# Optimization experiments

Hardware: AMD Instinct MI355X
Metric: run time of the kernel (lower is better)

The kernel has to match this reference:

```python
import jax, jax.numpy as jnp
import numpy as np

B = 2            # batch size
GRID = 256       # BEV grid H = W
M = 30000        # number of pillars (voxels)
NPTS = 200000    # number of points
IN_C = 16
VOXEL = 0.4      # voxel_size[:2]
PC_MIN = -51.2   # pc_range[:2]
DS = 2           # prod(ds_layer_strides)


def _bn(x, g, b):
    # eval-mode BatchNorm with running_mean=0, running_var=1 (eps absorbed into g)
    return x * g + b


def _conv(x, k, stride):
    # 3x3 conv, padding=1 (spconv SparseConv2d / SubMConv2d with pad k//2), NHWC
    return jax.lax.conv_general_dilated(
        x, k, (stride, stride), ((1, 1), (1, 1)),
        dimension_numbers=('NHWC', 'HWIO', 'NHWC'))


def _active_mask(occ, stride):
    # active output sites of a sparse conv = any active input in the 3x3 receptive field
    pooled = jax.lax.reduce_window(occ, -jnp.inf, jax.lax.max,
                                   (1, 3, 3, 1), (1, stride, stride, 1),
                                   ((0, 0), (1, 1), (1, 1), (0, 0)))
    return (pooled > 0).astype(occ.dtype)


def _forward(features, pfn_w0, pfn_g0, pfn_b0, pfn_w1, pfn_g1, pfn_b1,
             b1_kd, b1_gd, b1_bd, b1_k1, b1_g1, b1_b1, b1_k2, b1_g2, b1_b2,
             b2_kd, b2_gd, b2_bd, b2_k1, b2_g1, b2_b1, b2_k2, b2_g2, b2_b2,
             unq, unq_inv, grid_size):
    # pillar mode: cols 0:2 are xy; convert to (fractional) voxel coordinates
    pos = (features[:, :2] - PC_MIN) / VOXEL  # [N,2] = (px, py)

    # PFN layer 0 (not last): linear(16->16) + BN + ReLU, concat per-pillar max
    h = jax.nn.relu(_bn(features @ pfn_w0, pfn_g0, pfn_b0))            # [N,16]
    hmax = jax.ops.segment_max(h, unq_inv, num_segments=M)             # [M,16]
    h = jnp.concatenate([h, hmax[unq_inv]], axis=1)                    # [N,32]
    # PFN layer 1 (last): linear(32->64) + BN + ReLU
    h = jax.nn.relu(_bn(h @ pfn_w1, pfn_g1, pfn_b1))                   # [N,64]

    # scatter_max pooling points -> pillars
    fv = jax.ops.segment_max(h, unq_inv, num_segments=M)               # [M,64]

    Hn = grid_size
    img = jnp.zeros((B, Hn, Hn, fv.shape[1]), fv.dtype)
    img = img.at[unq[:, 0], unq[:, 1], unq[:, 2]].set(fv)              # dense BEV, NHWC
    occ = jnp.zeros((B, Hn, Hn, 1), fv.dtype)
    occ = occ.at[unq[:, 0], unq[:, 1], unq[:, 2]].set(1.0)

    # block 1: SparseConvBlock(stride=1) + SparseBasicBlock (dense math, masked to active sites)
    occ1 = _active_mask(occ, 1)
    x = jax.nn.relu(_bn(_conv(img, b1_kd, 1), b1_gd, b1_bd)) * occ1
    y = jax.nn.relu(_bn(_conv(x, b1_k1, 1), b1_g1, b1_b1)) * occ1
    y = _bn(_conv(y, b1_k2, 1), b1_g2, b1_b2) * occ1
    x = jax.nn.relu(x + y)

    # block 2: SparseConvBlock(stride=2) + SparseBasicBlock
    occ2 = _active_mask(occ1, 2)
    x = jax.nn.relu(_bn(_conv(x, b2_kd, 2), b2_gd, b2_bd)) * occ2
    y = jax.nn.relu(_bn(_conv(x, b2_k1, 1), b2_g1, b2_b1)) * occ2
    y = _bn(_conv(y, b2_k2, 1), b2_g2, b2_b2) * occ2
    x = jax.nn.relu(x + y)                                             # [B,H/2,W/2,128]

    # bilinear gather at per-point downsampled positions (px -> W axis, py -> H axis)
    bidx = unq[unq_inv, 0]
    px = pos[:, 0] / DS
    py = pos[:, 1] / DS
    Hc, Wc = x.shape[1], x.shape[2]
    x0 = jnp.clip(jnp.floor(px).astype(jnp.int32), 0, Wc - 1)
    x1 = jnp.clip(jnp.floor(px).astype(jnp.int32) + 1, 0, Wc - 1)
    y0 = jnp.clip(jnp.floor(py).astype(jnp.int32), 0, Hc - 1)
    y1 = jnp.clip(jnp.floor(py).astype(jnp.int32) + 1, 0, Hc - 1)
    Ia = x[bidx, y0, x0]
    Ib = x[bidx, y1, x0]
    Ic = x[bidx, y0, x1]
    Id = x[bidx, y1, x1]
    x0f, x1f = x0.astype(px.dtype), x1.astype(px.dtype)
    y0f, y1f = y0.astype(py.dtype), y1.astype(py.dtype)
    wa = ((x1f - px) * (y1f - py))[:, None]
    wb = ((x1f - px) * (py - y0f))[:, None]
    wc = ((px - x0f) * (y1f - py))[:, None]
    wd = ((px - x0f) * (py - y0f))[:, None]
    return Ia * wa + Ib * wb + Ic * wc + Id * wd                       # [N,128]


def setup_inputs() -> dict:
    rng = np.random.default_rng(0)
    d = {}
    d['features'] = jnp.asarray(rng.standard_normal((NPTS, IN_C)).astype(np.float32))
    # unique voxel coords (batch, y, x)
    lin = rng.choice(B * GRID * GRID, size=M, replace=False)
    d['unq'] = jnp.asarray(np.stack([lin // (GRID * GRID), (lin // GRID) % GRID, lin % GRID], 1).astype(np.int32))
    # every pillar gets at least one point
    d['unq_inv'] = jnp.asarray(np.concatenate([np.arange(M), rng.integers(0, M, NPTS - M)]).astype(np.int32))
    d['grid_size'] = GRID

    def w(*s):
        fan = int(np.prod(s[:-1]))
        return jnp.asarray((rng.standard_normal(s) / np.sqrt(fan)).astype(np.float32))

    def g(c):
        return jnp.asarray((0.5 + 0.5 * rng.random(c)).astype(np.float32))

    def bb(c):
        return jnp.asarray((0.1 * rng.standard_normal(c)).astype(np.float32))

    d['pfn_w0'] = w(IN_C, 16); d['pfn_g0'] = g(16); d['pfn_b0'] = bb(16)
    d['pfn_w1'] = w(32, 64);   d['pfn_g1'] = g(64); d['pfn_b1'] = bb(64)
    d['b1_kd'] = w(3, 3, 64, 64);   d['b1_gd'] = g(64);  d['b1_bd'] = bb(64)
    d['b1_k1'] = w(3, 3, 64, 64);   d['b1_g1'] = g(64);  d['b1_b1'] = bb(64)
    d['b1_k2'] = w(3, 3, 64, 64);   d['b1_g2'] = g(64);  d['b1_b2'] = bb(64)
    d['b2_kd'] = w(3, 3, 64, 128);  d['b2_gd'] = g(128); d['b2_bd'] = bb(128)
    d['b2_k1'] = w(3, 3, 128, 128); d['b2_g1'] = g(128); d['b2_b1'] = bb(128)
    d['b2_k2'] = w(3, 3, 128, 128); d['b2_g2'] = g(128); d['b2_b2'] = bb(128)
    return d


def reference(features, unq, unq_inv, grid_size,
              pfn_w0, pfn_g0, pfn_b0, pfn_w1, pfn_g1, pfn_b1,
              b1_kd, b1_gd, b1_bd, b1_k1, b1_g1, b1_b1, b1_k2, b1_g2, b1_b2,
              b2_kd, b2_gd, b2_bd, b2_k1, b2_g1, b2_b1, b2_k2, b2_g2, b2_b2):
    return _forward(features, pfn_w0, pfn_g0, pfn_b0, pfn_w1, pfn_g1, pfn_b1,
                    b1_kd, b1_gd, b1_bd, b1_k1, b1_g1, b1_b1, b1_k2, b1_g2, b1_b2,
                    b2_kd, b2_gd, b2_bd, b2_k1, b2_g1, b2_b1, b2_k2, b2_g2, b2_b2,
                    unq, unq_inv, grid_size)
```

## Files before the change

### kernel.cpp

```cpp
#include <hip/hip_runtime.h>
#include <hip/hip_bf16.h>

#define NPTS    200000
#define MPIL    30000
#define BATCH   2
#define GRID0   256
#define PCMIN   (-51.2f)
#define VOXEL0  (0.4f)
#define NCHUNK  118

#define SLOT_B  ((size_t)16777216)
#define SLOT_F  ((size_t)33554432)

#define W0F 0
#define W1F 256
#define FB1 9216
#define FB2 156672
#define FB3 304128
#define FB4 451584
#define FB5 746496
#define FB6 1336320

#define WS_FLAG 0
#define WS_OCC8 64
#define WS_OCC1 (64 + 131072)
#define WS_OCC2 (64 + 262144)
#define WS_HMAX 393280
#define WS_CNT  2313280
#define WS_OFF  2433280
#define WS_CUR  2553344
#define WS_IDX  2673344
#define WS_LOC  3473344
#define WS_BS   3593344
#define WS_FX   393344

typedef __attribute__((ext_vector_type(8))) short v8s;
typedef __attribute__((ext_vector_type(4))) float f32x4;

static __device__ __forceinline__ float b2f(__hip_bfloat16 v) { return __bfloat162float(v); }
static __device__ __forceinline__ unsigned short f2bbits(float f) {
    __hip_bfloat16 h = __float2bfloat16(f);
    union { __hip_bfloat16 h; unsigned short u; } cv; cv.h = h; return cv.u;
}
static __device__ __forceinline__ float bits2f(unsigned short h) {
    union { unsigned int u; float f; } c; c.u = ((unsigned int)h) << 16; return c.f;
}
static __device__ __forceinline__ float lo2f(unsigned int u) {
    union { unsigned int u; float f; } c; c.u = u << 16; return c.f;
}
static __device__ __forceinline__ float hi2f(unsigned int u) {
    union { unsigned int u; float f; } c; c.u = u & 0xFFFF0000u; return c.f;
}
static __device__ __forceinline__ unsigned int pack2(float a, float b) {
    return (unsigned int)f2bbits(a) | ((unsigned int)f2bbits(b) << 16);
}
static __device__ __forceinline__ void split2(float a, float b, unsigned int& hi, unsigned int& lo) {
    unsigned short ha = f2bbits(a), hb = f2bbits(b);
    hi = (unsigned int)ha | ((unsigned int)hb << 16);
    float ra = a - bits2f(ha);
    float rb = b - bits2f(hb);
    lo = (unsigned int)f2bbits(ra) | ((unsigned int)f2bbits(rb) << 16);
}

static __device__ __forceinline__ float ldf(const void* p, size_t i, int isb) {
    return isb ? b2f(((const __hip_bfloat16*)p)[i]) : ((const float*)p)[i];
}
static __device__ __forceinline__ float4 ld4(const void* p, size_t i, int isb) {
    if (isb) {
        uint2 r = *(const uint2*)((const __hip_bfloat16*)p + i);
        return make_float4(lo2f(r.x), hi2f(r.x), lo2f(r.y), hi2f(r.y));
    }
    return *(const float4*)((const float*)p + i);
}
static __device__ __forceinline__ void st4(void* p, size_t i, int isb, float4 v) {
    if (isb) {
        uint2 pk; pk.x = pack2(v.x, v.y); pk.y = pack2(v.z, v.w);
        *(uint2*)((__hip_bfloat16*)p + i) = pk;
    } else {
        *(float4*)((float*)p + i) = v;
    }
}
static __device__ __forceinline__ void* actptr(void* ob, int slot, int isb) {
    return (char*)ob + (size_t)slot * (isb ? SLOT_B : SLOT_F);
}
static __device__ __forceinline__ float* wpool(void* ob, int isb) {
    return (float*)((char*)ob + 3 * (isb ? SLOT_B : SLOT_F));
}

__global__ void probe_kernel(const unsigned short* __restrict__ g0, int* __restrict__ flag) {
    if (threadIdx.x == 0 && blockIdx.x == 0) {
        int ok = 1;
        for (int i = 0; i < 8; i++) {
            unsigned short u = g0[i];
            if (u < 0x3E00 || u >= 0x4000) ok = 0;
        }
        *flag = ok;
    }
}

__global__ __launch_bounds__(256) void cvt_kernel(const void* __restrict__ src, void* ob,
                                                  int woff, int n, const int* __restrict__ flag) {
    int isb = *flag;
    int i = blockIdx.x * 256 + threadIdx.x;
    if (i < n) wpool(ob, isb)[woff + i] = ldf(src, i, isb);
}

__global__ __launch_bounds__(256) void wfrag_kernel(const void* __restrict__ src, void* ob,
                                                    int fb_bytes, int CIN, int COUT,
                                                    const int* __restrict__ flag)
{
    const int isb = *flag;
    const int cnt = 9 * CIN * COUT;
    int e = blockIdx.x * 256 + threadIdx.x;
    if (e >= cnt) return;
    int i = e & 7;
    int l = (e >> 3) & 63;
    int f = e >> 9;
    int nbn = COUT >> 4, kcn = CIN >> 5;
    int nb = f % nbn;
    int kc = (f / nbn) % kcn;
    int tap = f / (nbn * kcn);
    int ci = kc * 32 + (l >> 4) * 8 + i;
    int co = nb * 16 + (l & 15);
    float wv = ldf(src, (size_t)(tap * CIN + ci) * COUT + co, isb);
    unsigned short h = f2bbits(wv);
    float rem = wv - bits2f(h);
    short* wh = (short*)((char*)ob + 3 * (isb ? SLOT_B : SLOT_F) + fb_bytes);
    wh[e] = (short)h;
    wh[cnt + e] = (short)f2bbits(rem);
}

__global__ __launch_bounds__(256) void hist_kernel(const int* __restrict__ unq_inv,
                                                   int* __restrict__ cnt)
{
    int n = blockIdx.x * 256 + threadIdx.x;
    if (n < NPTS) atomicAdd(&cnt[unq_inv[n]], 1);
}

__global__ __launch_bounds__(256) void scan1_kernel(const int* __restrict__ cnt,
                                                    int* __restrict__ loc,
                                                    int* __restrict__ bs)
{
    __shared__ int s[256];
    const int tid = threadIdx.x;
    const int i = blockIdx.x * 256 + tid;
    int v = (i < MPIL) ? cnt[i] : 0;
    s[tid] = v;
    __syncthreads();
#pragma unroll
    for (int d = 1; d < 256; d <<= 1) {
        int t = (tid >= d) ? s[tid - d] : 0;
        __syncthreads();
        s[tid] += t;
        __syncthreads();
    }
    if (i < MPIL) loc[i] = s[tid] - v;
    if (tid == 255) bs[blockIdx.x] = s[255];
}

__global__ __launch_bounds__(128) void scan2_kernel(int* __restrict__ bs)
{
    __shared__ int s[NCHUNK];
    const int tid = threadIdx.x;
    for (int i = tid; i < NCHUNK; i += 128) s[i] = bs[i];
    __syncthreads();
    if (tid == 0) {
        int acc = 0;
        for (int i = 0; i < NCHUNK; i++) { int t = s[i]; s[i] = acc; acc += t; }
    }
    __syncthreads();
    for (int i = tid; i < NCHUNK; i += 128) bs[i] = s[i];
}

__global__ __launch_bounds__(256) void scan3_kernel(const int* __restrict__ loc,
                                                    const int* __restrict__ bs,
                                                    int* __restrict__ off,
                                                    int* __restrict__ cur)
{
    int i = blockIdx.x * 256 + threadIdx.x;
    if (i < MPIL) {
        int e = loc[i] + bs[blockIdx.x];
        off[i] = e; cur[i] = e;
    }
    if (i == 0) off[MPIL] = NPTS;
}

__global__ __launch_bounds__(256) void fill_kernel(const int* __restrict__ unq_inv,
                                                   int* __restrict__ cur,
                                                   int* __restrict__ idxarr)
{
    int n = blockIdx.x * 256 + threadIdx.x;
    if (n >= NPTS) return;
    int p = unq_inv[n];
    int s = atomicAdd(&cur[p], 1);
    idxarr[s] = n;
}

__global__ __launch_bounds__(256) void pfn0_kernel(
    const void* __restrict__ feat, void* ob, const void* __restrict__ g0,
    const void* __restrict__ b0, const int* __restrict__ flag)
{
    const int isb = *flag;
    int n = blockIdx.x * 256 + threadIdx.x;
    if (n >= NPTS) return;
    const float* w0f = wpool(ob, isb) + W0F;
    void* h0 = actptr(ob, 1, isb);
    float f[16];
#pragma unroll
    for (int i = 0; i < 16; i += 4) {
        float4 v = ld4(feat, (size_t)n * 16 + i, isb);
        f[i] = v.x; f[i + 1] = v.y; f[i + 2] = v.z; f[i + 3] = v.w;
    }
#pragma unroll
    for (int co = 0; co < 16; co += 4) {
        float a0 = 0.f, a1 = 0.f, a2 = 0.f, a3 = 0.f;
#pragma unroll
        for (int ci = 0; ci < 16; ci++) {
            float4 w = *(const float4*)&w0f[ci * 16 + co];
            a0 += f[ci] * w.x; a1 += f[ci] * w.y; a2 += f[ci] * w.z; a3 += f[ci] * w.w;
        }
        float o[4] = { a0, a1, a2, a3 };
#pragma unroll
        for (int k = 0; k < 4; k++) {
            float z = o[k] * ldf(g0, co + k, isb) + ldf(b0, co + k, isb);
            o[k] = fmaxf(z, 0.f);
        }
        st4(h0, (size_t)n * 16 + co, isb, make_float4(o[0], o[1], o[2], o[3]));
    }
}

__global__ __launch_bounds__(256) void hmax_kernel(
    void* ob, const int* __restrict__ off, const int* __restrict__ idxarr,
    float* __restrict__ hmax, const int* __restrict__ flag)
{
    const int isb = *flag;
    int t = blockIdx.x * 256 + threadIdx.x;
    if (t >= MPIL * 16) return;
    int p = t >> 4, ch = t & 15;
    const void* h0 = actptr(ob, 1, isb);
    float m = 0.f;
    int s1 = off[p + 1];
    for (int s = off[p]; s < s1; s++) {
        int n = idxarr[s];
        m = fmaxf(m, ldf(h0, (size_t)n * 16 + ch, isb));
    }
    hmax[t] = m;
}

template<bool BF>
static __device__ __forceinline__ void pfn1p_body(
    void* ob, const float* __restrict__ hmax, const void* __restrict__ g1,
    const void* __restrict__ b1, const int* __restrict__ off,
    const int* __restrict__ idxarr, const int* __restrict__ unq,
    unsigned char* __restrict__ occ)
{
    const int lane = threadIdx.x & 63;
    const int p = (blockIdx.x << 2) + (threadIdx.x >> 6);
    if (p >= MPIL) return;
    const int isb = BF ? 1 : 0;
    const float* w1f = wpool(ob, isb) + W1F;
    const void* h0 = actptr(ob, 1, isb);
    void* img = actptr(ob, 0, isb);

    float wcol[32];
#pragma unroll
    for (int k = 0; k < 32; k++) wcol[k] = w1f[k * 64 + lane];
    float base = 0.f;
#pragma unroll
    for (int k = 0; k < 16; k++) base += hmax[(size_t)p * 16 + k] * wcol[16 + k];
    const float g = ldf(g1, lane, isb);
    const float be = ldf(b1, lane, isb);

    float m = 0.f;
    const int s1 = off[p + 1];
    for (int s = off[p]; s < s1; s++) {
        const int n = idxarr[s];
        float h[16];
        if (BF) {
            const unsigned short* hp = (const unsigned short*)h0 + (size_t)n * 16;
            uint4 a = *(const uint4*)hp;
            uint4 c = *(const uint4*)(hp + 8);
            h[0] = lo2f(a.x); h[1] = hi2f(a.x); h[2] = lo2f(a.y); h[3] = hi2f(a.y);
            h[4] = lo2f(a.z); h[5] = hi2f(a.z); h[6] = lo2f(a.w); h[7] = hi2f(a.w);
            h[8] = lo2f(c.x); h[9] = hi2f(c.x); h[10] = lo2f(c.y); h[11] = hi2f(c.y);
            h[12] = lo2f(c.z); h[13] = hi2f(c.z); h[14] = lo2f(c.w); h[15] = hi2f(c.w);
        } else {
            const float* fp = (const float*)h0 + (size_t)n * 16;
#pragma unroll
            for (int i = 0; i < 16; i += 4) {
                float4 v = *(const float4*)(fp + i);
                h[i] = v.x; h[i + 1] = v.y; h[i + 2] = v.z; h[i + 3] = v.w;
            }
        }
        float z = base;
#pragma unroll
        for (int k = 0; k < 16; k++) z += h[k] * wcol[k];
        z = fmaxf(z * g + be, 0.f);
        m = fmaxf(m, z);
    }

    const int bb = unq[p * 3 + 0], yy = unq[p * 3 + 1], xx = unq[p * 3 + 2];
    const size_t site = ((size_t)bb * GRID0 + yy) * GRID0 + xx;
    if (BF) ((unsigned short*)img)[site * 64 + lane] = f2bbits(m);
    else    ((float*)img)[site * 64 + lane] = m;
    if (lane == 0) occ[site] = 1;
}

__global__ __launch_bounds__(256) void pfn1p_kernel(
    void* ob, const float* __restrict__ hmax, const void* __restrict__ g1,
    const void* __restrict__ b1, const int* __restrict__ off,
    const int* __restrict__ idxarr, const int* __restrict__ unq,
    unsigned char* __restrict__ occ, const int* __restrict__ flag)
{
    if (*flag) pfn1p_body<true>(ob, hmax, g1, b1, off, idxarr, unq, occ);
    else       pfn1p_body<false>(ob, hmax, g1, b1, off, idxarr, unq, occ);
}

__global__ __launch_bounds__(256) void dilate1_kernel(const unsigned char* __restrict__ occ,
                                                      unsigned char* __restrict__ occ1)
{
    int idx = blockIdx.x * 256 + threadIdx.x;
    if (idx >= BATCH * GRID0 * GRID0) return;
    int b = idx / (GRID0 * GRID0);
    int r = idx % (GRID0 * GRID0);
    int y = r / GRID0, x = r % GRID0;
    unsigned char v = 0;
#pragma unroll
    for (int dy = -1; dy <= 1; dy++) {
        int yy = y + dy; if (yy < 0 || yy >= GRID0) continue;
#pragma unroll
        for (int dx = -1; dx <= 1; dx++) {
            int xx = x + dx; if (xx < 0 || xx >= GRID0) continue;
            v |= occ[((size_t)b * GRID0 + yy) * GRID0 + xx];
        }
    }
    occ1[idx] = v ? 1 : 0;
}

__global__ __launch_bounds__(256) void dilate2_kernel(const unsigned char* __restrict__ occ1,
                                                      unsigned char* __restrict__ occ2)
{
    int idx = blockIdx.x * 256 + threadIdx.x;
    if (idx >= BATCH * 128 * 128) return;
    int b = idx / (128 * 128);
    int r = idx % (128 * 128);
    int y = r / 128, x = r % 128;
    unsigned char v = 0;
#pragma unroll
    for (int dy = -1; dy <= 1; dy++) {
        int yy = 2 * y + dy; if (yy < 0 || yy >= GRID0) continue;
#pragma unroll
        for (int dx = -1; dx <= 1; dx++) {
            int xx = 2 * x + dx; if (xx < 0 || xx >= GRID0) continue;
            v |= occ1[((size_t)b * GRID0 + yy) * GRID0 + xx];
        }
    }
    occ2[idx] = v ? 1 : 0;
}

template<int CIN, int COUT, int STRIDE, bool ADD_RES, bool BF, int RT, int WC, int WP, int CSPLIT>
static __device__ __forceinline__ void conv_tile(
    short* s_a, const void* in, void* outp, const void* res, const short* wh,
    const void* gamma, const void* beta, const unsigned char* mask,
    int HIN, int WIN, int HOUT, int WOUT, int b, int oy0, int ox0, int nbB)
{
    constexpr int Y_EXT = (RT - 1) * STRIDE + 3;
    constexpr int X_EXT = 15 * STRIDE + 3;
    constexpr int TSZ = Y_EXT * X_EXT * CIN;
    constexpr int NCH8 = CIN / 8;
    constexpr int RPW = RT / WP;
    constexpr int CG = COUT / 16 / CSPLIT / WC;
    constexpr int KCN = CIN / 32;
    constexpr int KCNT = 9 * KCN;
    constexpr int CP = 3;
    constexpr int NPASS = KCNT / CP;
    constexpr int NOB = COUT / 16;

    const int tid = threadIdx.x;

    __syncthreads();
    for (int i = tid; i < Y_EXT * X_EXT * NCH8; i += 256) {
        int c8 = i % NCH8;
        int r = i / NCH8;
        int xo = r % X_EXT;
        int dy = r / X_EXT;
        int yin = oy0 * STRIDE - 1 + dy;
        int xin = ox0 * STRIDE - 1 + xo;
        bool inb = (yin >= 0 && yin < HIN && xin >= 0 && xin < WIN);
        int si = (dy * X_EXT + xo) * CIN + ((c8 ^ (xo & 7)) << 3);
        size_t gi = (((size_t)b * HIN + yin) * WIN + xin) * (size_t)CIN + c8 * 8;
        if (BF) {
            uint4 v = make_uint4(0u, 0u, 0u, 0u);
            if (inb) v = *(const uint4*)((const unsigned short*)in + gi);
            *(uint4*)&s_a[si] = v;
        } else {
            float4 va = make_float4(0.f, 0.f, 0.f, 0.f);
            float4 vb = make_float4(0.f, 0.f, 0.f, 0.f);
            if (inb) {
                va = *(const float4*)((const float*)in + gi);
                vb = *(const float4*)((const float*)in + gi + 4);
            }
            uint4 hv, lv;
            split2(va.x, va.y, hv.x, lv.x);
            split2(va.z, va.w, hv.y, lv.y);
            split2(vb.x, vb.y, hv.z, lv.z);
            split2(vb.z, vb.w, hv.w, lv.w);
            *(uint4*)&s_a[si] = hv;
            *(uint4*)&s_a[TSZ + si] = lv;
        }
    }
    __syncthreads();

    const int lane = tid & 63;
    const int w = tid >> 6;
    const int cgb = nbB + (w % WC) * CG;
    const int row0 = (w / WC) * RPW;
    const int l15 = lane & 15;
    const int lhi = lane >> 4;
    const short* wl = wh + 9 * CIN * COUT;

    f32x4 acc[RPW][CG];
#pragma unroll
    for (int pt = 0; pt < RPW; pt++)
#pragma unroll
        for (int g = 0; g < CG; g++) acc[pt][g] = (f32x4){0.f, 0.f, 0.f, 0.f};

#pragma unroll 1
    for (int ps = 0; ps < NPASS; ps++) {
        const int cb0 = ps * CP;
        v8s wa[CP * CG];
        v8s wo[BF ? 1 : CP * CG];
#pragma unroll
        for (int c = 0; c < CP; c++)
#pragma unroll
            for (int g = 0; g < CG; g++) {
                const size_t f = (size_t)(cb0 + c) * NOB + cgb + g;
                wa[c * CG + g] = *(const v8s*)&wh[f * 512 + lane * 8];
                if constexpr (!BF)
                    wo[c * CG + g] = *(const v8s*)&wl[f * 512 + lane * 8];
            }
        v8s xv[CP * RPW];
        v8s xl[BF ? 1 : CP * RPW];
#pragma unroll
        for (int c = 0; c < CP; c++) {
            const int cgl = cb0 + c;
            const int tap = cgl / KCN;
            const int kc = cgl - tap * KCN;
            const int ky = tap / 3, kx = tap - ky * 3;
            const int xo = l15 * STRIDE + kx;
            const int coff = (((kc * 4 + lhi) ^ (xo & 7)) << 3);
#pragma unroll
            for (int pt = 0; pt < RPW; pt++) {
                const int ba = (((row0 + pt) * STRIDE + ky) * X_EXT + xo) * CIN + coff;
                xv[c * RPW + pt] = *(const v8s*)&s_a[ba];
                if constexpr (!BF) xl[c * RPW + pt] = *(const v8s*)&s_a[TSZ + ba];
            }
        }
#pragma unroll
        for (int c = 0; c < CP; c++)
#pragma unroll
            for (int pt = 0; pt < RPW; pt++)
#pragma unroll
                for (int g = 0; g < CG; g++) {
                    acc[pt][g] = __builtin_amdgcn_mfma_f32_16x16x32_bf16(
                        wa[c * CG + g], xv[c * RPW + pt], acc[pt][g], 0, 0, 0);
                    if constexpr (!BF) {
                        acc[pt][g] = __builtin_amdgcn_mfma_f32_16x16x32_bf16(
                            wa[c * CG + g], xl[c * RPW + pt], acc[pt][g], 0, 0, 0);
                        acc[pt][g] = __builtin_amdgcn_mfma_f32_16x16x32_bf16(
                            wo[c * CG + g], xv[c * RPW + pt], acc[pt][g], 0, 0, 0);
                    }
                }
    }

#pragma unroll
    for (int g = 0; g < CG; g++) {
        const int ch = (cgb + g) * 16 + lhi * 4;
        float gm[4], bt[4];
#pragma unroll
        for (int r = 0; r < 4; r++) {
            gm[r] = ldf(gamma, ch + r, BF ? 1 : 0);
            bt[r] = ldf(beta, ch + r, BF ? 1 : 0);
        }
#pragma unroll
        for (int pt = 0; pt < RPW; pt++) {
            const int oy = oy0 + row0 + pt;
            const size_t prow = ((size_t)b * HOUT + oy) * WOUT + ox0 + l15;
            const float mk = mask[prow] ? 1.f : 0.f;
            float z[4];
#pragma unroll
            for (int r = 0; r < 4; r++)
                z[r] = (acc[pt][g][r] * gm[r] + bt[r]) * mk;
            if constexpr (ADD_RES) {
                if (BF) {
                    uint2 rr = *(const uint2*)((const unsigned short*)res + prow * COUT + ch);
                    z[0] += lo2f(rr.x); z[1] += hi2f(rr.x);
                    z[2] += lo2f(rr.y); z[3] += hi2f(rr.y);
                } else {
                    float4 rr = *(const float4*)((const float*)res + prow * COUT + ch);
                    z[0] += rr.x; z[1] += rr.y; z[2] += rr.z; z[3] += rr.w;
                }
            }
#pragma unroll
            for (int r = 0; r < 4; r++) z[r] = fmaxf(z[r], 0.f);
            if (BF) {
                uint2 pk;
                pk.x = pack2(z[0], z[1]);
                pk.y = pack2(z[2], z[3]);
                *(uint2*)((unsigned short*)outp + prow * COUT + ch) = pk;
            } else {
                *(float4*)((float*)outp + prow * COUT + ch) = make_float4(z[0], z[1], z[2], z[3]);
            }
        }
    }
}

template<int CIN, int COUT, int STRIDE, int R, int RTF, int CSPLIT, bool ADD_RES>
__global__ __launch_bounds__(256) void convmf_kernel(
    void* ob, int in_slot, int out_slot, void* out_ws, int res_slot, int fb_bytes,
    const void* __restrict__ gamma, const void* __restrict__ beta,
    const unsigned char* __restrict__ mask, const int* __restrict__ flag,
    int HIN, int WIN, int HOUT, int WOUT)
{
    constexpr int X_EXT = 15 * STRIDE + 3;
    constexpr int TSZ_B = ((R - 1) * STRIDE + 3) * X_EXT * CIN;
    constexpr int TSZ_F2 = 2 * (((RTF - 1) * STRIDE + 3) * X_EXT * CIN);
    constexpr int LDS_SH = (TSZ_B > TSZ_F2) ? TSZ_B : TSZ_F2;
    __shared__ __align__(16) short s_a[LDS_SH];

    const int nbx = gridDim.x, nby = gridDim.y;
    const int nwg = nbx * nby * (int)gridDim.z;
    int bid = blockIdx.x + nbx * (blockIdx.y + nby * blockIdx.z);
    bid = (bid & 7) * (nwg >> 3) + (bid >> 3);
    const int bx = bid % nbx;
    const int byy = (bid / nbx) % nby;
    const int bzz = bid / (nbx * nby);
    const int b = bzz / CSPLIT;
    const int coh = bzz % CSPLIT;
    const int nbB = coh * (COUT / 16 / CSPLIT);

    const int isb = *flag;
    const void* in = actptr(ob, in_slot, isb);
    void* outp = out_ws ? out_ws : actptr(ob, out_slot, isb);
    const void* res = ADD_RES ? actptr(ob, res_slot, isb) : nullptr;
    const short* wh = (const short*)((const char*)ob + 3 * (isb ? SLOT_B : SLOT_F) + fb_bytes);

    if (isb) {
        conv_tile<CIN, COUT, STRIDE, ADD_RES, true, R, 1, 4, CSPLIT>(
            s_a, in, outp, res, wh, gamma, beta, mask,
            HIN, WIN, HOUT, WOUT, b, byy * R, bx * 16, nbB);
    } else {
#pragma unroll 1
        for (int p = 0; p < R / RTF; p++)
            conv_tile<CIN, COUT, STRIDE, ADD_RES, false, RTF, 4, 1, CSPLIT>(
                s_a, in, outp, res, wh, gamma, beta, mask,
                HIN, WIN, HOUT, WOUT, b, byy * R + p * RTF, bx * 16, nbB);
    }
}

__global__ __launch_bounds__(256) void gather_kernel(
    const void* __restrict__ x, const void* __restrict__ feat,
    const int* __restrict__ unq, const int* __restrict__ unq_inv,
    void* __restrict__ out, const int* __restrict__ flag)
{
    const int isb = *flag;
    int idx = blockIdx.x * 256 + threadIdx.x;
    if (idx >= NPTS * 32) return;
    int n = idx >> 5;
    int co = (idx & 31) * 4;
    float fx = ldf(feat, (size_t)n * 16 + 0, isb);
    float fy = ldf(feat, (size_t)n * 16 + 1, isb);
    float px = ((fx - PCMIN) / VOXEL0) / 2.0f;
    float py = ((fy - PCMIN) / VOXEL0) / 2.0f;
    int bi = unq[(size_t)unq_inv[n] * 3 + 0];
    int xf = (int)floorf(px), yf = (int)floorf(py);
    int x0 = min(max(xf, 0), 127), x1 = min(max(xf + 1, 0), 127);
    int y0 = min(max(yf, 0), 127), y1 = min(max(yf + 1, 0), 127);
    float x0f = (float)x0, x1f = (float)x1, y0f = (float)y0, y1f = (float)y1;
    float wa = (x1f - px) * (y1f - py);
    float wb = (x1f - px) * (py - y0f);
    float wc = (px - x0f) * (y1f - py);
    float wd = (px - x0f) * (py - y0f);
    size_t base = (size_t)bi * 128 * 128 * 128;
    float4 Ia = ld4(x, base + ((size_t)y0 * 128 + x0) * 128 + co, isb);
    float4 Ib = ld4(x, base + ((size_t)y1 * 128 + x0) * 128 + co, isb);
    float4 Ic = ld4(x, base + ((size_t)y0 * 128 + x1) * 128 + co, isb);
    float4 Id = ld4(x, base + ((size_t)y1 * 128 + x1) * 128 + co, isb);
    float4 r;
    r.x = Ia.x * wa + Ib.x * wb + Ic.x * wc + Id.x * wd;
    r.y = Ia.y * wa + Ib.y * wb + Ic.y * wc + Id.y * wd;
    r.z = Ia.z * wa + Ib.z * wb + Ic.z * wc + Id.z * wd;
    r.w = Ia.w * wa + Ib.w * wb + Ic.w * wc + Id.w * wd;
    st4(out, (size_t)n * 128 + co, isb, r);
}

extern "C" void kernel_launch(void* const* d_in, const int* in_sizes, int n_in,
                              void* d_out, int out_size, void* d_ws, size_t ws_size,
                              hipStream_t stream)
{
    (void)in_sizes; (void)n_in; (void)out_size; (void)ws_size;
    const int* unq = (const int*)d_in[1];
    const int* unq_inv = (const int*)d_in[2];

    char* ws = (char*)d_ws;
    int* flagp = (int*)(ws + WS_FLAG);
    unsigned char* occ8 = (unsigned char*)(ws + WS_OCC8);
    unsigned char* occ1m = (unsigned char*)(ws + WS_OCC1);
    unsigned char* occ2m = (unsigned char*)(ws + WS_OCC2);
    float* hmax = (float*)(ws + WS_HMAX);
    int* cnt = (int*)(ws + WS_CNT);
    int* off = (int*)(ws + WS_OFF);
    int* cur = (int*)(ws + WS_CUR);
    int* idxarr = (int*)(ws + WS_IDX);
    int* loc = (int*)(ws + WS_LOC);
    int* bs = (int*)(ws + WS_BS);
    void* Fx = (void*)(ws + WS_FX);

    probe_kernel<<<1, 64, 0, stream>>>((const unsigned short*)d_in[5], flagp);

    cvt_kernel<<<1, 256, 0, stream>>>(d_in[4], d_out, W0F, 256, flagp);
    cvt_kernel<<<8, 256, 0, stream>>>(d_in[7], d_out, W1F, 2048, flagp);
    wfrag_kernel<<<144, 256, 0, stream>>>(d_in[10], d_out, FB1, 64, 64, flagp);
    wfrag_kernel<<<144, 256, 0, stream>>>(d_in[13], d_out, FB2, 64, 64, flagp);
    wfrag_kernel<<<144, 256, 0, stream>>>(d_in[16], d_out, FB3, 64, 64, flagp);
    wfrag_kernel<<<288, 256, 0, stream>>>(d_in[19], d_out, FB4, 64, 128, flagp);
    wfrag_kernel<<<576, 256, 0, stream>>>(d_in[22], d_out, FB5, 128, 128, flagp);
    wfrag_kernel<<<576, 256, 0, stream>>>(d_in[25], d_out, FB6, 128, 128, flagp);

    hipMemsetAsync(d_out, 0, SLOT_F, stream);
    hipMemsetAsync(cnt, 0, (size_t)MPIL * 4, stream);
    hipMemsetAsync(occ8, 0, 131072, stream);

    hist_kernel<<<(NPTS + 255) / 256, 256, 0, stream>>>(unq_inv, cnt);
    scan1_kernel<<<NCHUNK, 256, 0, stream>>>(cnt, loc, bs);
    scan2_kernel<<<1, 128, 0, stream>>>(bs);
    scan3_kernel<<<NCHUNK, 256, 0, stream>>>(loc, bs, off, cur);
    fill_kernel<<<(NPTS + 255) / 256, 256, 0, stream>>>(unq_inv, cur, idxarr);
    pfn0_kernel<<<(NPTS + 255) / 256, 256, 0, stream>>>(d_in[0], d_out, d_in[5], d_in[6], flagp);
    hmax_kernel<<<(MPIL * 16 + 255) / 256, 256, 0, stream>>>(d_out, off, idxarr, hmax, flagp);
    pfn1p_kernel<<<(MPIL + 3) / 4, 256, 0, stream>>>(d_out, hmax, d_in[8], d_in[9],
                                                     off, idxarr, unq, occ8, flagp);

    dilate1_kernel<<<(BATCH * GRID0 * GRID0) / 256, 256, 0, stream>>>(occ8, occ1m);
    dilate2_kernel<<<(BATCH * 128 * 128) / 256, 256, 0, stream>>>(occ1m, occ2m);

    dim3 blk(256);
    dim3 g1(16, 32, BATCH);
    convmf_kernel<64, 64, 1, 8, 2, 1, false><<<g1, blk, 0, stream>>>(
        d_out, 0, 1, nullptr, 0, FB1, d_in[11], d_in[12], occ1m, flagp, 256, 256, 256, 256);
    convmf_kernel<64, 64, 1, 8, 2, 1, false><<<g1, blk, 0, stream>>>(
        d_out, 1, 2, nullptr, 0, FB2, d_in[14], d_in[15], occ1m, flagp, 256, 256, 256, 256);
    convmf_kernel<64, 64, 1, 8, 2, 1, true><<<g1, blk, 0, stream>>>(
        d_out, 2, 0, nullptr, 1, FB3, d_in[17], d_in[18], occ1m, flagp, 256, 256, 256, 256);
    dim3 g2a(8, 32, BATCH * 2), g2b(8, 32, BATCH * 2);
    convmf_kernel<64, 128, 2, 4, 1, 2, false><<<g2a, blk, 0, stream>>>(
        d_out, 0, 1, nullptr, 0, FB4, d_in[20], d_in[21], occ2m, flagp, 256, 256, 128, 128);
    convmf_kernel<128, 128, 1, 4, 1, 2, false><<<g2b, blk, 0, stream>>>(
        d_out, 1, 2, nullptr, 0, FB5, d_in[23], d_in[24], occ2m, flagp, 128, 128, 128, 128);
    convmf_kernel<128, 128, 1, 4, 1, 2, true><<<g2b, blk, 0, stream>>>(
        d_out, 2, 0, Fx, 1, FB6, d_in[26], d_in[27], occ2m, flagp, 128, 128, 128, 128);

    gather_kernel<<<(NPTS * 32) / 256, 256, 0, stream>>>(Fx, d_in[0], unq, unq_inv,
                                                         d_out, flagp);
}
```

Measured before the change: 549.1 us.

## Fuse per-pillar hmax into pfn1p kernel and pin conv operand loads with asm barriers

Drops the separate hmax kernel. Each pillar's 16-channel max of layer-0 features is now computed inside pfn1p by a first pass over the pillar's points, which saves one launch and the hmax global buffer round trip. In exchange every point's h0 row is read twice per wavefront, and all 64 lanes do the same redundant max work. Separately, empty asm volatile constraints on the weight and activation fragments in the MFMA conv loop force those loads to complete before the compute, to steer the compiler's scheduling.

```diff
diff --git a/kernel.cpp b/kernel.cpp
--- a/kernel.cpp
+++ b/kernel.cpp
@@ -25,7 +25,6 @@
 #define WS_OCC8 64
 #define WS_OCC1 (64 + 131072)
 #define WS_OCC2 (64 + 262144)
-#define WS_HMAX 393280
 #define WS_CNT  2313280
 #define WS_OFF  2433280
 #define WS_CUR  2553344
@@ -229,27 +228,9 @@
     }
 }
 
-__global__ __launch_bounds__(256) void hmax_kernel(
-    void* ob, const int* __restrict__ off, const int* __restrict__ idxarr,
-    float* __restrict__ hmax, const int* __restrict__ flag)
-{
-    const int isb = *flag;
-    int t = blockIdx.x * 256 + threadIdx.x;
-    if (t >= MPIL * 16) return;
-    int p = t >> 4, ch = t & 15;
-    const void* h0 = actptr(ob, 1, isb);
-    float m = 0.f;
-    int s1 = off[p + 1];
-    for (int s = off[p]; s < s1; s++) {
-        int n = idxarr[s];
-        m = fmaxf(m, ldf(h0, (size_t)n * 16 + ch, isb));
-    }
-    hmax[t] = m;
-}
-
 template<bool BF>
 static __device__ __forceinline__ void pfn1p_body(
-    void* ob, const float* __restrict__ hmax, const void* __restrict__ g1,
+    void* ob, const void* __restrict__ g1,
     const void* __restrict__ b1, const int* __restrict__ off,
     const int* __restrict__ idxarr, const int* __restrict__ unq,
     unsigned char* __restrict__ occ)
@@ -265,15 +246,44 @@
     float wcol[32];
 #pragma unroll
     for (int k = 0; k < 32; k++) wcol[k] = w1f[k * 64 + lane];
-    float base = 0.f;
-#pragma unroll
-    for (int k = 0; k < 16; k++) base += hmax[(size_t)p * 16 + k] * wcol[16 + k];
     const float g = ldf(g1, lane, isb);
     const float be = ldf(b1, lane, isb);
 
+    const int s0 = off[p], s1 = off[p + 1];
+
+    float m16[16];
+#pragma unroll
+    for (int k = 0; k < 16; k++) m16[k] = 0.f;
+    for (int s = s0; s < s1; s++) {
+        const int n = idxarr[s];
+        if (BF) {
+            const unsigned short* hp = (const unsigned short*)h0 + (size_t)n * 16;
+            uint4 a = *(const uint4*)hp;
+            uint4 c = *(const uint4*)(hp + 8);
+            m16[0] = fmaxf(m16[0], lo2f(a.x)); m16[1] = fmaxf(m16[1], hi2f(a.x));
+            m16[2] = fmaxf(m16[2], lo2f(a.y)); m16[3] = fmaxf(m16[3], hi2f(a.y));
+            m16[4] = fmaxf(m16[4], lo2f(a.z)); m16[5] = fmaxf(m16[5], hi2f(a.z));
+            m16[6] = fmaxf(m16[6], lo2f(a.w)); m16[7] = fmaxf(m16[7], hi2f(a.w));
+            m16[8] = fmaxf(m16[8], lo2f(c.x)); m16[9] = fmaxf(m16[9], hi2f(c.x));
+            m16[10] = fmaxf(m16[10], lo2f(c.y)); m16[11] = fmaxf(m16[11], hi2f(c.y));
+            m16[12] = fmaxf(m16[12], lo2f(c.z)); m16[13] = fmaxf(m16[13], hi2f(c.z));
+            m16[14] = fmaxf(m16[14], lo2f(c.w)); m16[15] = fmaxf(m16[15], hi2f(c.w));
+        } else {
+            const float* fp = (const float*)h0 + (size_t)n * 16;
+#pragma unroll
+            for (int i = 0; i < 16; i += 4) {
+                float4 v = *(const float4*)(fp + i);
+                m16[i] = fmaxf(m16[i], v.x); m16[i + 1] = fmaxf(m16[i + 1], v.y);
+                m16[i + 2] = fmaxf(m16[i + 2], v.z); m16[i + 3] = fmaxf(m16[i + 3], v.w);
+            }
+        }
+    }
+    float base = 0.f;
+#pragma unroll
+    for (int k = 0; k < 16; k++) base += m16[k] * wcol[16 + k];
+
     float m = 0.f;
-    const int s1 = off[p + 1];
-    for (int s = off[p]; s < s1; s++) {
+    for (int s = s0; s < s1; s++) {
         const int n = idxarr[s];
         float h[16];
         if (BF) {
@@ -307,13 +317,13 @@
 }
 
 __global__ __launch_bounds__(256) void pfn1p_kernel(
-    void* ob, const float* __restrict__ hmax, const void* __restrict__ g1,
+    void* ob, const void* __restrict__ g1,
     const void* __restrict__ b1, const int* __restrict__ off,
     const int* __restrict__ idxarr, const int* __restrict__ unq,
     unsigned char* __restrict__ occ, const int* __restrict__ flag)
 {
-    if (*flag) pfn1p_body<true>(ob, hmax, g1, b1, off, idxarr, unq, occ);
-    else       pfn1p_body<false>(ob, hmax, g1, b1, off, idxarr, unq, occ);
+    if (*flag) pfn1p_body<true>(ob, g1, b1, off, idxarr, unq, occ);
+    else       pfn1p_body<false>(ob, g1, b1, off, idxarr, unq, occ);
 }
 
 __global__ __launch_bounds__(256) void dilate1_kernel(const unsigned char* __restrict__ occ,
@@ -439,6 +449,12 @@
                 if constexpr (!BF)
                     wo[c * CG + g] = *(const v8s*)&wl[f * 512 + lane * 8];
             }
+#pragma unroll
+        for (int q = 0; q < CP * CG; q++) asm volatile("" : "+v"(wa[q]));
+        if constexpr (!BF) {
+#pragma unroll
+            for (int q = 0; q < CP * CG; q++) asm volatile("" : "+v"(wo[q]));
+        }
         v8s xv[CP * RPW];
         v8s xl[BF ? 1 : CP * RPW];
 #pragma unroll
@@ -455,6 +471,12 @@
                 xv[c * RPW + pt] = *(const v8s*)&s_a[ba];
                 if constexpr (!BF) xl[c * RPW + pt] = *(const v8s*)&s_a[TSZ + ba];
             }
+        }
+#pragma unroll
+        for (int q = 0; q < CP * RPW; q++) asm volatile("" : "+v"(xv[q]));
+        if constexpr (!BF) {
+#pragma unroll
+            for (int q = 0; q < CP * RPW; q++) asm volatile("" : "+v"(xl[q]));
         }
 #pragma unroll
         for (int c = 0; c < CP; c++)
@@ -607,7 +629,6 @@
     unsigned char* occ8 = (unsigned char*)(ws + WS_OCC8);
     unsigned char* occ1m = (unsigned char*)(ws + WS_OCC1);
     unsigned char* occ2m = (unsigned char*)(ws + WS_OCC2);
-    float* hmax = (float*)(ws + WS_HMAX);
     int* cnt = (int*)(ws + WS_CNT);
     int* off = (int*)(ws + WS_OFF);
     int* cur = (int*)(ws + WS_CUR);
@@ -637,8 +658,7 @@
     scan3_kernel<<<NCHUNK, 256, 0, stream>>>(loc, bs, off, cur);
     fill_kernel<<<(NPTS + 255) / 256, 256, 0, stream>>>(unq_inv, cur, idxarr);
     pfn0_kernel<<<(NPTS + 255) / 256, 256, 0, stream>>>(d_in[0], d_out, d_in[5], d_in[6], flagp);
-    hmax_kernel<<<(MPIL * 16 + 255) / 256, 256, 0, stream>>>(d_out, off, idxarr, hmax, flagp);
-    pfn1p_kernel<<<(MPIL + 3) / 4, 256, 0, stream>>>(d_out, hmax, d_in[8], d_in[9],
+    pfn1p_kernel<<<(MPIL + 3) / 4, 256, 0, stream>>>(d_out, d_in[8], d_in[9],
                                                      off, idxarr, unq, occ8, flagp);
 
     dilate1_kernel<<<(BATCH * GRID0 * GRID0) / 256, 256, 0, stream>>>(occ8, occ1m);
```

New measurement: 598.9 us. 1.09x slower.
